# Kernel tuning notes

Measured on AMD Instinct MI355X. Metric: run time of the kernel, lower is better.

The kernel has to match this reference:

```python
import jax, jax.numpy as jnp
import numpy as np

N, E, F, L, G, C = 100000, 1600000, 128, 3, 512, 40
BN_EPS = 1e-5


def gcn_conv(x, src, dst, W, b, n_nodes):
    # PyG GCNConv: linear transform, symmetric normalization with self-loops,
    # scatter-add aggregation, then bias.
    xw = x @ W                                   # [N, H]
    deg = jnp.zeros((n_nodes,), x.dtype).at[dst].add(1.0) + 1.0  # +1 self-loop
    dinv = jax.lax.rsqrt(deg)                    # D^{-1/2}
    norm = dinv[src] * dinv[dst]                 # [E]
    msg = xw[src] * norm[:, None]                # gather + scale, [E, H]
    agg = jnp.zeros_like(xw).at[dst].add(msg)    # scatter-add to destinations
    agg = agg + xw * (dinv * dinv)[:, None]      # self-loop contribution
    return agg + b


def setup_inputs() -> dict:
    key = jax.random.key(0)
    ks = jax.random.split(key, 6)
    x = jax.random.normal(ks[0], (N, F), dtype=jnp.float32)
    edge_index = jax.random.randint(ks[1], (2, E), 0, N, dtype=jnp.int64)
    batch = jnp.sort(jax.random.randint(ks[2], (N,), 0, G, dtype=jnp.int64))
    conv_w = jax.random.normal(ks[3], (L, F, F), dtype=jnp.float32) * 0.05
    conv_b = jnp.zeros((L, F), dtype=jnp.float32)
    bn_gamma = jnp.ones((L, F), dtype=jnp.float32)
    bn_beta = jnp.zeros((L, F), dtype=jnp.float32)
    bn_mean = jnp.zeros((L, F), dtype=jnp.float32)
    bn_var = jnp.ones((L, F), dtype=jnp.float32)
    lin_w = jax.random.normal(ks[4], (F, C), dtype=jnp.float32) * 0.05
    lin_b = jnp.zeros((C,), dtype=jnp.float32)
    return {"x": x, "edge_index": edge_index, "batch": batch,
            "conv_w": conv_w, "conv_b": conv_b,
            "bn_gamma": bn_gamma, "bn_beta": bn_beta,
            "bn_mean": bn_mean, "bn_var": bn_var,
            "lin_w": lin_w, "lin_b": lin_b}


def reference(x, edge_index, batch, conv_w, conv_b, bn_gamma, bn_beta,
              bn_mean, bn_var, lin_w, lin_b):
    src, dst = edge_index[0], edge_index[1]
    h = x
    # layers 0..L-2: conv -> BN(eval) -> ReLU (dropout is identity in eval)
    for i in range(L - 1):
        h = gcn_conv(h, src, dst, conv_w[i], conv_b[i], N)
        h = (h - bn_mean[i]) * (bn_gamma[i] * jax.lax.rsqrt(bn_var[i] + BN_EPS)) + bn_beta[i]
        h = jax.nn.relu(h)
    # last conv (no BN/ReLU)
    h = gcn_conv(h, src, dst, conv_w[L - 1], conv_b[L - 1], N)
    # global_mean_pool over graphs
    sums = jnp.zeros((G, F), h.dtype).at[batch].add(h)
    counts = jnp.zeros((G,), h.dtype).at[batch].add(1.0)
    pooled = sums / jnp.maximum(counts, 1.0)[:, None]   # [G, F]
    return pooled @ lin_w + lin_b                        # [G, C]
```

## Files before the change

### kernel.cpp

```cpp
#include <hip/hip_runtime.h>

#define Nn 100000
#define Ee 1600000
#define Ff 128
#define Gg 512
#define Cc 40
#define NB 1563
#define PAD 32
#define FB 256
#define EPB 6250

__global__ void prep_scales_k(const float* __restrict__ conv_b,
                              const float* __restrict__ gamma,
                              const float* __restrict__ beta,
                              const float* __restrict__ mean,
                              const float* __restrict__ var,
                              float* __restrict__ sc, float* __restrict__ sh)
{
    int i = blockIdx.x * blockDim.x + threadIdx.x;
    if (i >= 3 * Ff) return;
    float b = conv_b[i];
    if (i < 2 * Ff) {
        float s = gamma[i] * rsqrtf(var[i] + 1e-5f);
        sc[i] = s;
        sh[i] = (b - mean[i]) * s + beta[i];
    } else {
        sc[i] = 1.0f;
        sh[i] = b;
    }
}

__global__ __launch_bounds__(1024) void bucket_count_k(
    const int* __restrict__ dst, int* __restrict__ bcnt)
{
    __shared__ int cnt[NB];
    const int t = threadIdx.x;
    for (int b = t; b < NB; b += 1024) cnt[b] = 0;
    __syncthreads();
    const int e0 = blockIdx.x * EPB;
    #pragma unroll
    for (int j = 0; j < 7; ++j) {
        int e = e0 + t + j * 1024;
        if (e < e0 + EPB) atomicAdd(&cnt[dst[e] >> 6], 1);
    }
    __syncthreads();
    for (int b = t; b < NB; b += 1024) {
        int c = cnt[b];
        if (c) atomicAdd(&bcnt[b * PAD], c);
    }
}

__global__ void scan_buckets_k(const int* __restrict__ bcnt, int* __restrict__ bktOff,
                               int* __restrict__ off)
{
    __shared__ int tot[256];
    int t = threadIdx.x;
    int v[7]; int s = 0;
    #pragma unroll
    for (int j = 0; j < 7; ++j) {
        int idx = t * 7 + j;
        int val = (idx < NB) ? bcnt[idx * PAD] : 0;
        v[j] = val; s += val;
    }
    tot[t] = s;
    __syncthreads();
    for (int d = 1; d < 256; d <<= 1) {
        int x = (t >= d) ? tot[t - d] : 0;
        __syncthreads();
        tot[t] += x;
        __syncthreads();
    }
    int base = tot[t] - s;
    #pragma unroll
    for (int j = 0; j < 7; ++j) {
        int idx = t * 7 + j;
        if (idx < NB) bktOff[idx] = base;
        base += v[j];
    }
    if (t == 255) { bktOff[NB] = base; off[Nn] = base; }
}

__global__ __launch_bounds__(1024) void bucket_fill_k(
    const int* __restrict__ src, const int* __restrict__ dst,
    const int* __restrict__ bktOff, int* __restrict__ bcur,
    int* __restrict__ staged)
{
    __shared__ int cnt[NB];
    __shared__ int gb[NB];
    const int t = threadIdx.x;
    for (int b = t; b < NB; b += 1024) cnt[b] = 0;
    __syncthreads();
    const int e0 = blockIdx.x * EPB;
    int bb[7], lp[7], pl[7];
    #pragma unroll
    for (int j = 0; j < 7; ++j) {
        int e = e0 + t + j * 1024;
        bb[j] = -1;
        if (e < e0 + EPB) {
            int d = dst[e];
            int b = d >> 6;
            bb[j] = b;
            lp[j] = atomicAdd(&cnt[b], 1);
            pl[j] = src[e] | ((d & 63) << 17);
        }
    }
    __syncthreads();
    for (int b = t; b < NB; b += 1024) {
        int c = cnt[b];
        gb[b] = c ? atomicAdd(&bcur[b * PAD], c) : 0;
    }
    __syncthreads();
    #pragma unroll
    for (int j = 0; j < 7; ++j) {
        int b = bb[j];
        if (b >= 0) staged[bktOff[b] + gb[b] + lp[j]] = pl[j];
    }
}

__global__ __launch_bounds__(256) void bucket_scatter_k(
    const int* __restrict__ staged, const int* __restrict__ bktOff,
    int* __restrict__ off, float* __restrict__ dinv, int* __restrict__ csrc)
{
    __shared__ int cl[64], ol[64], cu[64];
    const int b = blockIdx.x, tid = threadIdx.x;
    const int base = bktOff[b], base2 = bktOff[b + 1];
    if (tid < 64) cl[tid] = 0;
    __syncthreads();
    for (int i = base + tid; i < base2; i += 256)
        atomicAdd(&cl[staged[i] >> 17], 1);
    __syncthreads();
    if (tid == 0) {
        int r = 0;
        #pragma unroll
        for (int l = 0; l < 64; ++l) { ol[l] = r; r += cl[l]; }
    }
    __syncthreads();
    if (tid < 64) {
        int node = b * 64 + tid;
        if (node < Nn) {
            off[node]  = base + ol[tid];
            dinv[node] = rsqrtf((float)cl[tid] + 1.0f);
        }
        cu[tid] = 0;
    }
    __syncthreads();
    for (int i = base + tid; i < base2; i += 256) {
        int w = staged[i];
        int l = w >> 17;
        int pos = atomicAdd(&cu[l], 1);
        csrc[base + ol[l] + pos] = w & 0x1FFFF;
    }
}

__global__ __launch_bounds__(256) void gemm_scale_k(
    const float* __restrict__ A, const float* __restrict__ W,
    const float* __restrict__ dinv, float* __restrict__ Y, int n)
{
    const int tid  = threadIdx.x;
    const int half = __builtin_amdgcn_readfirstlane(tid >> 7);
    const int cb   = half * 64;
    const int r    = blockIdx.x * 128 + (tid & 127);
    const int rr   = min(r, n - 1);
    const float4* Ap = (const float4*)(A + ((size_t)rr << 7));
    const float*  Wp = W + cb;

    float acc[64];
    #pragma unroll
    for (int c = 0; c < 64; ++c) acc[c] = 0.f;

    for (int kc = 0; kc < 4; ++kc) {
        float4 a[8];
        #pragma unroll
        for (int i = 0; i < 8; ++i) a[i] = Ap[kc * 8 + i];
        const float* af = reinterpret_cast<const float*>(a);
        #pragma unroll
        for (int kk = 0; kk < 32; ++kk) {
            const float av = af[kk];
            const float* wr = Wp + (kc * 32 + kk) * Ff;
            #pragma unroll
            for (int c = 0; c < 64; ++c)
                acc[c] = fmaf(av, wr[c], acc[c]);
        }
    }

    if (r < n) {
        const float di = dinv[r];
        float* yp = Y + ((size_t)r << 7) + cb;
        #pragma unroll
        for (int c = 0; c < 64; c += 4)
            *(float4*)(yp + c) = make_float4(acc[c] * di, acc[c + 1] * di,
                                             acc[c + 2] * di, acc[c + 3] * di);
    }
}

__global__ __launch_bounds__(256) void aggregate_k(
    const float* __restrict__ Y, const int* __restrict__ off,
    const int* __restrict__ srcs, const float* __restrict__ dinv,
    const float* __restrict__ sc, const float* __restrict__ sh,
    float* __restrict__ H, int dorelu, int n)
{
    int wid  = threadIdx.x >> 6;
    int lane = threadIdx.x & 63;
    int node = blockIdx.x * 4 + wid;
    if (node >= n) return;
    int beg = off[node], end = off[node + 1];
    int c = lane * 2;

    float2 self = *(const float2*)(Y + (size_t)node * Ff + c);
    float ax = self.x, ay = self.y;
    float bx = 0.f,    by = 0.f;

    for (int e = beg; e < end; e += 64) {
        int nb = min(64, end - e);
        int sidx = (lane < nb) ? srcs[e + lane] : 0;
        int j = 0;
        for (; j + 4 <= nb; j += 4) {
            int s0 = __shfl(sidx, j);
            int s1 = __shfl(sidx, j + 1);
            int s2 = __shfl(sidx, j + 2);
            int s3 = __shfl(sidx, j + 3);
            float2 v0 = *(const float2*)(Y + (size_t)s0 * Ff + c);
            float2 v1 = *(const float2*)(Y + (size_t)s1 * Ff + c);
            float2 v2 = *(const float2*)(Y + (size_t)s2 * Ff + c);
            float2 v3 = *(const float2*)(Y + (size_t)s3 * Ff + c);
            ax += v0.x; ay += v0.y; bx += v1.x; by += v1.y;
            ax += v2.x; ay += v2.y; bx += v3.x; by += v3.y;
        }
        for (; j < nb; ++j) {
            int s0 = __shfl(sidx, j);
            float2 v0 = *(const float2*)(Y + (size_t)s0 * Ff + c);
            ax += v0.x; ay += v0.y;
        }
    }
    float di = dinv[node];
    float2 scv = *(const float2*)(sc + c);
    float2 shv = *(const float2*)(sh + c);
    float ox = (ax + bx) * di * scv.x + shv.x;
    float oy = (ay + by) * di * scv.y + shv.y;
    if (dorelu) { ox = fmaxf(ox, 0.f); oy = fmaxf(oy, 0.f); }
    *(float2*)(H + (size_t)node * Ff + c) = make_float2(ox, oy);
}

__global__ __launch_bounds__(128) void pool_linear_k(
    const float* __restrict__ H, const int* __restrict__ batch,
    const float* __restrict__ lw, const float* __restrict__ lb,
    float* __restrict__ out)
{
    int g = blockIdx.x, f = threadIdx.x;
    int lo = 0, hi = Nn;
    while (lo < hi) { int m = (lo + hi) >> 1; if (batch[m] < g) lo = m + 1; else hi = m; }
    int start = lo;
    hi = Nn;
    while (lo < hi) { int m = (lo + hi) >> 1; if (batch[m] < g + 1) lo = m + 1; else hi = m; }
    int end = lo;

    float a0 = 0.f, a1 = 0.f, a2 = 0.f, a3 = 0.f;
    int i = start;
    for (; i + 4 <= end; i += 4) {
        a0 += H[(size_t)(i + 0) * Ff + f];
        a1 += H[(size_t)(i + 1) * Ff + f];
        a2 += H[(size_t)(i + 2) * Ff + f];
        a3 += H[(size_t)(i + 3) * Ff + f];
    }
    for (; i < end; ++i) a0 += H[(size_t)i * Ff + f];
    int cnt = end - start;
    __shared__ float pooled[Ff];
    pooled[f] = ((a0 + a1) + (a2 + a3)) / (float)max(cnt, 1);
    __syncthreads();
    if (f < Cc) {
        float o = lb[f];
        #pragma unroll 8
        for (int k = 0; k < Ff; ++k) o += pooled[k] * lw[k * Cc + f];
        out[g * Cc + f] = o;
    }
}

extern "C" void kernel_launch(void* const* d_in, const int* in_sizes, int n_in,
                              void* d_out, int out_size, void* d_ws, size_t ws_size,
                              hipStream_t stream)
{
    const float* x      = (const float*)d_in[0];
    const int*   ei     = (const int*)d_in[1];
    const int*   batch  = (const int*)d_in[2];
    const float* conv_w = (const float*)d_in[3];
    const float* conv_b = (const float*)d_in[4];
    const float* gamma  = (const float*)d_in[5];
    const float* beta   = (const float*)d_in[6];
    const float* mean   = (const float*)d_in[7];
    const float* var    = (const float*)d_in[8];
    const float* lw     = (const float*)d_in[9];
    const float* lb     = (const float*)d_in[10];
    float* out = (float*)d_out;

    const int* srcp = ei;
    const int* dstp = ei + Ee;

    float* h      = (float*)d_ws;
    float* y      = h + (size_t)Nn * Ff;
    float* dinv   = y + (size_t)Nn * Ff;
    float* sc     = dinv + Nn;
    float* sh     = sc + 3 * Ff;
    int*   bcnt   = (int*)(sh + 3 * Ff);
    int*   bcur   = bcnt + NB * PAD;
    int*   off    = bcur + NB * PAD;
    int*   csrc   = off + (Nn + 1);
    int*   bktOff = csrc + Ee;
    int*   staged = (int*)y;

    hipMemsetAsync(bcnt, 0, (size_t)(2 * NB * PAD) * sizeof(int), stream);

    prep_scales_k<<<2, 256, 0, stream>>>(conv_b, gamma, beta, mean, var, sc, sh);
    bucket_count_k<<<FB, 1024, 0, stream>>>(dstp, bcnt);
    scan_buckets_k<<<1, 256, 0, stream>>>(bcnt, bktOff, off);
    bucket_fill_k<<<FB, 1024, 0, stream>>>(srcp, dstp, bktOff, bcur, staged);
    bucket_scatter_k<<<NB, 256, 0, stream>>>(staged, bktOff, off, dinv, csrc);

    const int gemm_grid = (Nn + 127) / 128;
    const int agg_grid  = (Nn + 3) / 4;
    for (int l = 0; l < 3; ++l) {
        const float* in = (l == 0) ? x : h;
        gemm_scale_k<<<gemm_grid, 256, 0, stream>>>(in, conv_w + (size_t)l * Ff * Ff,
                                                    dinv, y, Nn);
        aggregate_k<<<agg_grid, 256, 0, stream>>>(
            y, off, csrc, dinv, sc + l * Ff, sh + l * Ff,
            h, (l < 2) ? 1 : 0, Nn);
    }
    pool_linear_k<<<Gg, 128, 0, stream>>>(h, batch, lw, lb, out);
}
```

Before: 733.2 us.

## Rewrite node GEMM as persistent row-loop with register-resident weight slices

The per-layer dense transform now launches a fixed grid of persistent blocks. Each thread keeps a 32x2 slice of the weight matrix in registers and loops over rows in a grid-stride pattern. Partial dot products are reduced across the K-groups with lane shuffles, and one quarter of the lanes write the dinv-scaled outputs. This replaces the old scheme, where each thread held 64 accumulators and streamed weights through scalar loads for one row. The aim is to stop reloading weights for every 128-row tile. The cost is that each iteration handles a single row, so global-load latency per row may be exposed, and shuffle reductions plus partly idle lanes are added.

```diff
diff --git a/kernel.cpp b/kernel.cpp
--- a/kernel.cpp
+++ b/kernel.cpp
@@ -9,6 +9,7 @@
 #define PAD 32
 #define FB 256
 #define EPB 6250
+#define GB 2048
 
 __global__ void prep_scales_k(const float* __restrict__ conv_b,
                               const float* __restrict__ gamma,
@@ -156,40 +157,43 @@
     const float* __restrict__ A, const float* __restrict__ W,
     const float* __restrict__ dinv, float* __restrict__ Y, int n)
 {
-    const int tid  = threadIdx.x;
-    const int half = __builtin_amdgcn_readfirstlane(tid >> 7);
-    const int cb   = half * 64;
-    const int r    = blockIdx.x * 128 + (tid & 127);
-    const int rr   = min(r, n - 1);
-    const float4* Ap = (const float4*)(A + ((size_t)rr << 7));
-    const float*  Wp = W + cb;
-
-    float acc[64];
-    #pragma unroll
-    for (int c = 0; c < 64; ++c) acc[c] = 0.f;
-
-    for (int kc = 0; kc < 4; ++kc) {
+    const int tid = threadIdx.x;
+    const int wv  = tid >> 6;
+    const int l   = tid & 63;
+    const int kg  = l >> 4;
+    const int cg  = l & 15;
+    const int k0  = kg * 32;
+    const int c0  = wv * 32 + cg * 2;
+
+    float2 wreg[32];
+    #pragma unroll
+    for (int j = 0; j < 32; ++j)
+        wreg[j] = *(const float2*)(W + (size_t)(k0 + j) * Ff + c0);
+
+    for (int r = blockIdx.x; r < n; r += GB) {
+        const float4* ap = (const float4*)(A + (size_t)r * Ff + k0);
         float4 a[8];
         #pragma unroll
-        for (int i = 0; i < 8; ++i) a[i] = Ap[kc * 8 + i];
+        for (int i = 0; i < 8; ++i) a[i] = ap[i];
         const float* af = reinterpret_cast<const float*>(a);
+
+        float p0 = 0.f, p1 = 0.f, q0 = 0.f, q1 = 0.f;
         #pragma unroll
-        for (int kk = 0; kk < 32; ++kk) {
-            const float av = af[kk];
-            const float* wr = Wp + (kc * 32 + kk) * Ff;
-            #pragma unroll
-            for (int c = 0; c < 64; ++c)
-                acc[c] = fmaf(av, wr[c], acc[c]);
-        }
-    }
-
-    if (r < n) {
-        const float di = dinv[r];
-        float* yp = Y + ((size_t)r << 7) + cb;
-        #pragma unroll
-        for (int c = 0; c < 64; c += 4)
-            *(float4*)(yp + c) = make_float4(acc[c] * di, acc[c + 1] * di,
-                                             acc[c + 2] * di, acc[c + 3] * di);
+        for (int j = 0; j < 32; j += 2) {
+            const float av0 = af[j], av1 = af[j + 1];
+            p0 = fmaf(av0, wreg[j].x, p0);
+            p1 = fmaf(av0, wreg[j].y, p1);
+            q0 = fmaf(av1, wreg[j + 1].x, q0);
+            q1 = fmaf(av1, wreg[j + 1].y, q1);
+        }
+        float r0 = p0 + q0, r1 = p1 + q1;
+        r0 += __shfl_xor(r0, 16); r0 += __shfl_xor(r0, 32);
+        r1 += __shfl_xor(r1, 16); r1 += __shfl_xor(r1, 32);
+
+        if (l < 16) {
+            const float di = dinv[r];
+            *(float2*)(Y + (size_t)r * Ff + c0) = make_float2(r0 * di, r1 * di);
+        }
     }
 }
 
@@ -315,12 +319,11 @@
     bucket_fill_k<<<FB, 1024, 0, stream>>>(srcp, dstp, bktOff, bcur, staged);
     bucket_scatter_k<<<NB, 256, 0, stream>>>(staged, bktOff, off, dinv, csrc);
 
-    const int gemm_grid = (Nn + 127) / 128;
-    const int agg_grid  = (Nn + 3) / 4;
+    const int agg_grid = (Nn + 3) / 4;
     for (int l = 0; l < 3; ++l) {
         const float* in = (l == 0) ? x : h;
-        gemm_scale_k<<<gemm_grid, 256, 0, stream>>>(in, conv_w + (size_t)l * Ff * Ff,
-                                                    dinv, y, Nn);
+        gemm_scale_k<<<GB, 256, 0, stream>>>(in, conv_w + (size_t)l * Ff * Ff,
+                                             dinv, y, Nn);
         aggregate_k<<<agg_grid, 256, 0, stream>>>(
             y, off, csrc, dinv, sc + l * Ff, sh + l * Ff,
             h, (l < 2) ? 1 : 0, Nn);
```

After: 907.2 us. +23.7%, slower.
